# Kernel tuning notes

Hardware: AMD Instinct MI355X
Metric: run time of the kernel (lower is better)

The kernel has to match this reference:

```python
import jax, jax.numpy as jnp
import numpy as np

KEY_DIM, VALUE_DIM, NUM_HEAD, OUT_DIM = 128, 64, 4, 64
HEAD_KDIM = KEY_DIM // NUM_HEAD   # 32
HEAD_VDIM = VALUE_DIM // NUM_HEAD # 16

def _xavier(key, shape):
    # xavier_uniform over (fan_in=shape[0], fan_out=prod(shape[1:])) like torch
    fan_in, fan_out = shape[0], int(np.prod(shape[1:]))
    lim = float(np.sqrt(6.0 / (fan_in + fan_out)))
    return jax.random.uniform(key, shape, jnp.float32, -lim, lim)

def setup_inputs() -> dict:
    key = jax.random.key(0)
    ks = jax.random.split(key, 7)
    B, Q, K = 2, 4096, 4096
    return {
        "q_data": jax.random.normal(ks[0], (B, Q, KEY_DIM), jnp.float32),
        "m_data": jax.random.normal(ks[1], (B, K, VALUE_DIM), jnp.float32),
        "mask": jax.random.randint(ks[2], (B, K), 0, 2, jnp.int32),
        "q_weights": _xavier(ks[3], (KEY_DIM, NUM_HEAD, HEAD_KDIM)),
        "k_weights": _xavier(ks[4], (VALUE_DIM, NUM_HEAD, HEAD_KDIM)),
        "v_weights": _xavier(ks[5], (VALUE_DIM, NUM_HEAD, HEAD_VDIM)),
        "o_weights": _xavier(ks[6], (NUM_HEAD, HEAD_VDIM, OUT_DIM)),
        "o_bias": jnp.zeros((OUT_DIM,), jnp.float32),
    }

def reference(q_data, m_data, mask, q_weights, k_weights, v_weights, o_weights, o_bias):
    head_kdim = q_weights.shape[-1]
    scale = head_kdim ** (-0.5)
    Q = jnp.einsum('bqa,ahc->bqhc', q_data, q_weights) * scale
    K = jnp.einsum('bka,ahc->bkhc', m_data, k_weights)
    V = jnp.einsum('bka,ahc->bkhc', m_data, v_weights)
    logits = jnp.einsum('bqhc,bkhc->bhqk', Q, K)
    neg = jnp.finfo(logits.dtype).min
    logits = jnp.where(mask[:, None, None, :] == 0, neg, logits)
    weights = jax.nn.softmax(logits, axis=-1)
    weight_avg = jnp.einsum('bhqk,bkhc->bqhc', weights, V)
    return jnp.einsum('bqhc,hco->bqo', weight_avg, o_weights) + o_bias
```

## Files before the change

kernel.cpp:

```cpp
#include <hip/hip_runtime.h>
#include <stdint.h>

#define B_  2
#define QN  4096
#define KN  4096
#define AD  128
#define MD  64
#define H_  4
#define C_  32
#define CV  16
#define OD  64

typedef short bf16x8 __attribute__((ext_vector_type(8)));
typedef short bf16x4 __attribute__((ext_vector_type(4)));
typedef float f32x4  __attribute__((ext_vector_type(4)));

__device__ __forceinline__ short f2bf(float f) {
  union { float f; unsigned u; } v; v.f = f;
  unsigned r = v.u + 0x7fffu + ((v.u >> 16) & 1u);
  return (short)(r >> 16);
}
__device__ __forceinline__ unsigned pack2t(float a, float b) {
  union { float f; unsigned u; } ua, ub; ua.f = a; ub.f = b;
  return __builtin_amdgcn_perm(ub.u, ua.u, 0x07060302u);
}
__device__ __forceinline__ bf16x4 pack4t(f32x4 p) {
  union { unsigned u[2]; bf16x4 v; } t;
  t.u[0] = pack2t(p[0], p[1]); t.u[1] = pack2t(p[2], p[3]);
  return t.v;
}
__device__ __forceinline__ bf16x8 cvt8(f32x4 a, f32x4 b) {
  bf16x8 o;
  o[0]=f2bf(a[0]); o[1]=f2bf(a[1]); o[2]=f2bf(a[2]); o[3]=f2bf(a[3]);
  o[4]=f2bf(b[0]); o[5]=f2bf(b[1]); o[6]=f2bf(b[2]); o[7]=f2bf(b[3]);
  return o;
}

__global__ __launch_bounds__(256) void k_proj(const float* __restrict__ qdf, const float* __restrict__ mdf,
                                              const float* __restrict__ qwf, const float* __restrict__ kwf,
                                              const float* __restrict__ vwf,
                                              const int* __restrict__ mask, int* __restrict__ kc,
                                              short* __restrict__ Qp, short* __restrict__ Kp,
                                              short* __restrict__ Vpt) {
  const int lane = threadIdx.x & 63;
  const int wid = threadIdx.x >> 6;
  const int n = lane & 15, quad = lane >> 4;
  const f32x4 z4 = {0.f,0.f,0.f,0.f};
  if (blockIdx.x < 1024) {
    const int t = blockIdx.x*4 + wid;
    const int rt = t >> 3, ct = t & 7;
    const int row = rt*16 + n;
    const int hc0 = ct*16;
    f32x4 acc = z4;
    #pragma unroll
    for (int ak = 0; ak < 4; ++ak) {
      const int a0 = ak*32 + quad*8;
      const float* ap = qdf + row*AD + a0;
      bf16x8 afrag = cvt8(*(const f32x4*)ap, *(const f32x4*)(ap + 4));
      bf16x8 bfrag;
      #pragma unroll
      for (int j = 0; j < 8; ++j) bfrag[j] = f2bf(qwf[(a0 + j)*128 + hc0 + n]);
      acc = __builtin_amdgcn_mfma_f32_16x16x32_bf16(afrag, bfrag, acc, 0, 0, 0);
    }
    const int h = hc0 >> 5, c0 = (hc0 & 31) + n;
    const float s = 0.17677669529663687f * 1.44269504088896341f;
    #pragma unroll
    for (int r = 0; r < 4; ++r) {
      const int rr = rt*16 + quad*4 + r;
      const int bb = rr >> 12, q = rr & 4095;
      Qp[((bb*H_ + h)*QN + q)*C_ + c0] = f2bf(acc[r] * s);
    }
    return;
  }
  __shared__ unsigned long long balS[64];
  __shared__ int pref[64];
  __shared__ int kcS;
  const int bidx = blockIdx.x - 1024;
  const int b = (bidx*4) / 3072;
  #pragma unroll
  for (int p = 0; p < 16; ++p) {
    const int seg = wid*16 + p;
    const unsigned long long bal = __ballot(mask[b*KN + seg*64 + lane] != 0);
    if (lane == 0) balS[seg] = bal;
  }
  __syncthreads();
  if (wid == 0) {
    int v = __popcll(balS[lane]); int incl = v;
    for (int d = 1; d < 64; d <<= 1) { int o = __shfl_up(incl, d); if (lane >= d) incl += o; }
    pref[lane] = incl - v;
    if (lane == 63) kcS = incl;
  }
  __syncthreads();
  const int Kc = kcS;
  const int nch = (Kc + 31) >> 5;
  const int t = bidx*4 + wid;
  const int rem = t - b*3072;
  const int rt = rem / 12, ct = rem - rt*12;
  if (rem == 0 && lane == 0) kc[b] = Kc;
  if (rt*16 >= nch*32) return;
  const int j = rt*16 + n;
  const int valid = (j < Kc);
  int src = 0;
  if (valid) {
    int seg = 0;
    #pragma unroll
    for (int st = 32; st >= 1; st >>= 1)
      if (seg + st < 64 && pref[seg + st] <= j) seg += st;
    int r2 = j - pref[seg];
    unsigned long long m = balS[seg];
    int pos = 0;
    #pragma unroll
    for (int w = 32; w >= 1; w >>= 1) {
      const int c = __popcll(m & ((1ull << w) - 1ull));
      if (r2 >= c) { r2 -= c; m >>= w; pos += w; }
    }
    src = seg*64 + pos;
  }
  const float* mrow = mdf + (b*KN + src)*MD;
  const int hc = ct*16 + n;
  f32x4 acc = z4;
  #pragma unroll
  for (int ch = 0; ch < 2; ++ch) {
    const int a0 = ch*32 + quad*8;
    bf16x8 afrag = cvt8(*(const f32x4*)(mrow + a0), *(const f32x4*)(mrow + a0 + 4));
    if (!valid) {
      #pragma unroll
      for (int jj = 0; jj < 8; ++jj) afrag[jj] = 0;
    }
    bf16x8 bfrag;
    if (ct < 8) {
      #pragma unroll
      for (int jj = 0; jj < 8; ++jj) bfrag[jj] = f2bf(kwf[(a0 + jj)*128 + hc]);
    } else {
      #pragma unroll
      for (int jj = 0; jj < 8; ++jj) bfrag[jj] = f2bf(vwf[(a0 + jj)*64 + hc - 128]);
    }
    acc = __builtin_amdgcn_mfma_f32_16x16x32_bf16(afrag, bfrag, acc, 0, 0, 0);
  }
  if (ct < 8) {
    const int h = hc >> 5, c = hc & 31;
    #pragma unroll
    for (int r = 0; r < 4; ++r) {
      const int jj2 = rt*16 + quad*4 + r;
      Kp[((b*H_ + h)*KN + jj2)*C_ + c] = f2bf(acc[r]);
    }
  } else {
    const int hc2 = hc - 128; const int h = hc2 >> 4, cv = hc2 & 15;
    bf16x4 pk; pk[0]=f2bf(acc[0]); pk[1]=f2bf(acc[1]); pk[2]=f2bf(acc[2]); pk[3]=f2bf(acc[3]);
    *(bf16x4*)(Vpt + ((b*H_ + h)*CV + cv)*KN + rt*16 + quad*4) = pk;
  }
}

__global__ __launch_bounds__(1024) void k_attn(const short* __restrict__ Qp, const short* __restrict__ Kp,
                                               const short* __restrict__ Vpt, const int* __restrict__ kc,
                                               const float* __restrict__ w2f, const float* __restrict__ obf,
                                               float* __restrict__ out) {
  __shared__ __attribute__((aligned(16))) char pool[40960];
  const int lane = threadIdx.x & 63, wid = threadIdx.x >> 6;
  const int h = wid & 3, split = wid >> 2;
  const int flatq = blockIdx.x * 32;
  const int b = flatq >> 12, qt = flatq & 4095;
  const int bh = b*H_ + h;
  const int n = lane & 15, quad = lane >> 4;
  const short* Qb = Qp + (bh*QN + qt)*C_;
  const short* Kb = Kp + bh*KN*C_;
  const short* Vb = Vpt + bh*CV*KN;
  const bf16x8 qb0 = *(const bf16x8*)(Qb + n*C_ + quad*8);
  const bf16x8 qb1 = *(const bf16x8*)(Qb + (16 + n)*C_ + quad*8);
  const int Kc = kc[b];
  const int nch = (Kc + 31) >> 5;
  const f32x4 z4 = {0.f,0.f,0.f,0.f};
  f32x4 o0 = z4, o1 = z4;
  float l0 = 0.f, l1 = 0.f;
  short* Pw = (short*)(pool + wid*2560);
  bf16x8 kf0, kf1, va;
  int ci = split;
  if (ci < nch) {
    const int kb = ci*32;
    kf0 = *(const bf16x8*)(Kb + (kb + n)*C_ + quad*8);
    kf1 = *(const bf16x8*)(Kb + (kb + 16 + n)*C_ + quad*8);
    va  = *(const bf16x8*)(Vb + n*KN + kb + quad*8);
  }
  for (; ci < nch; ci += 4) {
    const bf16x8 ckf0 = kf0, ckf1 = kf1, cva = va;
    const int cin = ci + 4;
    if (cin < nch) {
      const int kb2 = cin*32;
      kf0 = *(const bf16x8*)(Kb + (kb2 + n)*C_ + quad*8);
      kf1 = *(const bf16x8*)(Kb + (kb2 + 16 + n)*C_ + quad*8);
      va  = *(const bf16x8*)(Vb + n*KN + kb2 + quad*8);
    }
    f32x4 s00 = __builtin_amdgcn_mfma_f32_16x16x32_bf16(ckf0, qb0, z4, 0, 0, 0);
    f32x4 s01 = __builtin_amdgcn_mfma_f32_16x16x32_bf16(ckf0, qb1, z4, 0, 0, 0);
    f32x4 s10 = __builtin_amdgcn_mfma_f32_16x16x32_bf16(ckf1, qb0, z4, 0, 0, 0);
    f32x4 s11 = __builtin_amdgcn_mfma_f32_16x16x32_bf16(ckf1, qb1, z4, 0, 0, 0);
    f32x4 p00, p01, p10, p11;
    #pragma unroll
    for (int r = 0; r < 4; ++r) {
      p00[r] = __builtin_amdgcn_exp2f(s00[r]);
      p01[r] = __builtin_amdgcn_exp2f(s01[r]);
      p10[r] = __builtin_amdgcn_exp2f(s10[r]);
      p11[r] = __builtin_amdgcn_exp2f(s11[r]);
    }
    l0 += ((p00[0]+p00[1])+(p00[2]+p00[3])) + ((p10[0]+p10[1])+(p10[2]+p10[3]));
    l1 += ((p01[0]+p01[1])+(p01[2]+p01[3])) + ((p11[0]+p11[1])+(p11[2]+p11[3]));
    *(bf16x4*)(Pw + n*40 + quad*4)           = pack4t(p00);
    *(bf16x4*)(Pw + n*40 + 16 + quad*4)      = pack4t(p10);
    *(bf16x4*)(Pw + (16+n)*40 + quad*4)      = pack4t(p01);
    *(bf16x4*)(Pw + (16+n)*40 + 16 + quad*4) = pack4t(p11);
    const bf16x8 pb0 = *(const bf16x8*)(Pw + n*40 + quad*8);
    const bf16x8 pb1 = *(const bf16x8*)(Pw + (16+n)*40 + quad*8);
    o0 = __builtin_amdgcn_mfma_f32_16x16x32_bf16(cva, pb0, o0, 0, 0, 0);
    o1 = __builtin_amdgcn_mfma_f32_16x16x32_bf16(cva, pb1, o1, 0, 0, 0);
  }
  __syncthreads();
  float* Of   = (float*)pool;
  float* Lb   = (float*)(pool + 33280);
  short* ObfA = (short*)(pool + 35328);
  #pragma unroll
  for (int r = 0; r < 4; ++r) {
    const int hc = h*16 + quad*4 + r;
    Of[split*2080 + n*65 + hc]        = o0[r];
    Of[split*2080 + (16+n)*65 + hc]   = o1[r];
  }
  l0 += __shfl_xor(l0, 16); l0 += __shfl_xor(l0, 32);
  l1 += __shfl_xor(l1, 16); l1 += __shfl_xor(l1, 32);
  if (lane < 16) {
    Lb[split*128 + h*32 + lane]      = l0;
    Lb[split*128 + h*32 + 16 + lane] = l1;
  }
  __syncthreads();
  {
    const float npad = (float)(nch*32 - Kc);
    const int e = threadIdx.x * 2;
    const int q = e >> 6, hc = e & 63;
    const int hh = hc >> 4;
    const float l = (Lb[hh*32 + q] + Lb[128 + hh*32 + q])
                  + (Lb[256 + hh*32 + q] + Lb[384 + hh*32 + q]) - npad;
    const float inv = 1.00135f / l;
    const float v0 = ((Of[q*65 + hc]     + Of[2080 + q*65 + hc])
                    + (Of[4160 + q*65 + hc] + Of[6240 + q*65 + hc])) * inv;
    const float v1 = ((Of[q*65 + hc + 1] + Of[2080 + q*65 + hc + 1])
                    + (Of[4160 + q*65 + hc + 1] + Of[6240 + q*65 + hc + 1])) * inv;
    union { unsigned u; short s[2]; } pk;
    pk.s[0] = f2bf(v0); pk.s[1] = f2bf(v1);
    *(unsigned*)(ObfA + q*72 + hc) = pk.u;
  }
  __syncthreads();
  if (wid < 8) {
    const int mt = wid & 1, nt = wid >> 1;
    f32x4 acc = z4;
    #pragma unroll
    for (int kchunk = 0; kchunk < 2; ++kchunk) {
      const bf16x8 afrag = *(const bf16x8*)(ObfA + (mt*16 + n)*72 + kchunk*32 + quad*8);
      bf16x8 bfrag;
      #pragma unroll
      for (int jj = 0; jj < 8; ++jj)
        bfrag[jj] = f2bf(w2f[(kchunk*32 + quad*8 + jj)*64 + nt*16 + n]);
      acc = __builtin_amdgcn_mfma_f32_16x16x32_bf16(afrag, bfrag, acc, 0, 0, 0);
    }
    const int ocol = nt*16 + n;
    const float bias = obf[ocol];
    #pragma unroll
    for (int r = 0; r < 4; ++r) {
      const int qg = flatq + mt*16 + quad*4 + r;
      out[qg*64 + ocol] = acc[r] + bias;
    }
  }
}

extern "C" void kernel_launch(void* const* d_in, const int* in_sizes, int n_in,
                              void* d_out, int out_size, void* d_ws, size_t ws_size,
                              hipStream_t stream) {
  const float* qd  = (const float*)d_in[0];
  const float* md  = (const float*)d_in[1];
  const int*   msk = (const int*)  d_in[2];
  const float* qw  = (const float*)d_in[3];
  const float* kw  = (const float*)d_in[4];
  const float* vw  = (const float*)d_in[5];
  const float* ow  = (const float*)d_in[6];
  const float* ob  = (const float*)d_in[7];
  float* out = (float*)d_out;

  char* ws = (char*)d_ws;
  int*   kc  = (int*)  (ws);
  short* Qp  = (short*)(ws + (64<<10));
  short* Kp  = (short*)(ws + (64<<10) + (2u<<20));
  short* Vpt = (short*)(ws + (64<<10) + (4u<<20));

  hipLaunchKernelGGL(k_proj, dim3(2560), dim3(256),  0, stream, qd, md, qw, kw, vw, msk, kc, Qp, Kp, Vpt);
  hipLaunchKernelGGL(k_attn, dim3(256),  dim3(1024), 0, stream, Qp, Kp, Vpt, kc, ow, ob, out);
}
```

Before: 103.2 us.

## Fuse projection and attention into one cooperative kernel with grid sync

Measured after the change: 145.9 us. +41.5%, slower.

```diff
diff --git a/kernel.cpp b/kernel.cpp
--- a/kernel.cpp
+++ b/kernel.cpp
@@ -1,4 +1,5 @@
 #include <hip/hip_runtime.h>
+#include <hip/hip_cooperative_groups.h>
 #include <stdint.h>
 
 #define B_  2
@@ -36,21 +37,34 @@
   return o;
 }
 
-__global__ __launch_bounds__(256) void k_proj(const float* __restrict__ qdf, const float* __restrict__ mdf,
-                                              const float* __restrict__ qwf, const float* __restrict__ kwf,
-                                              const float* __restrict__ vwf,
-                                              const int* __restrict__ mask, int* __restrict__ kc,
-                                              short* __restrict__ Qp, short* __restrict__ Kp,
-                                              short* __restrict__ Vpt) {
-  const int lane = threadIdx.x & 63;
-  const int wid = threadIdx.x >> 6;
+__global__ __launch_bounds__(1024) void k_fused(
+    const float* __restrict__ qdf, const float* __restrict__ mdf,
+    const float* __restrict__ qwf, const float* __restrict__ kwf,
+    const float* __restrict__ vwf, const int* __restrict__ mask,
+    short* __restrict__ Kp, short* __restrict__ Vpt,
+    const float* __restrict__ w2f, const float* __restrict__ obf,
+    float* __restrict__ out) {
+  __shared__ __attribute__((aligned(16))) char pool[40960];
+  __shared__ __attribute__((aligned(16))) short QL[32*136];
+  __shared__ unsigned long long balS[64];
+  __shared__ int pref[64];
+  __shared__ int kcS;
+  const int lane = threadIdx.x & 63, wid = threadIdx.x >> 6;
   const int n = lane & 15, quad = lane >> 4;
+  const int bid = blockIdx.x;
+  const int flatq = bid * 32;
+  const int b = bid >> 7;
   const f32x4 z4 = {0.f,0.f,0.f,0.f};
-  if (blockIdx.x < 1024) {
-    const int t = blockIdx.x*4 + wid;
-    const int rt = t >> 3, ct = t & 7;
-    const int row = rt*16 + n;
-    const int hc0 = ct*16;
+
+  #pragma unroll
+  for (int p = 0; p < 4; ++p) {
+    const int seg = wid*4 + p;
+    const unsigned long long bal = __ballot(mask[b*KN + seg*64 + lane] != 0);
+    if (lane == 0) balS[seg] = bal;
+  }
+  {
+    const int mt = wid & 1, ct = wid >> 1;
+    const int row = flatq + mt*16 + n;
     f32x4 acc = z4;
     #pragma unroll
     for (int ak = 0; ak < 4; ++ak) {
@@ -59,29 +73,13 @@
       bf16x8 afrag = cvt8(*(const f32x4*)ap, *(const f32x4*)(ap + 4));
       bf16x8 bfrag;
       #pragma unroll
-      for (int j = 0; j < 8; ++j) bfrag[j] = f2bf(qwf[(a0 + j)*128 + hc0 + n]);
+      for (int j = 0; j < 8; ++j) bfrag[j] = f2bf(qwf[(a0 + j)*128 + ct*16 + n]);
       acc = __builtin_amdgcn_mfma_f32_16x16x32_bf16(afrag, bfrag, acc, 0, 0, 0);
     }
-    const int h = hc0 >> 5, c0 = (hc0 & 31) + n;
     const float s = 0.17677669529663687f * 1.44269504088896341f;
     #pragma unroll
-    for (int r = 0; r < 4; ++r) {
-      const int rr = rt*16 + quad*4 + r;
-      const int bb = rr >> 12, q = rr & 4095;
-      Qp[((bb*H_ + h)*QN + q)*C_ + c0] = f2bf(acc[r] * s);
-    }
-    return;
-  }
-  __shared__ unsigned long long balS[64];
-  __shared__ int pref[64];
-  __shared__ int kcS;
-  const int bidx = blockIdx.x - 1024;
-  const int b = (bidx*4) / 3072;
-  #pragma unroll
-  for (int p = 0; p < 16; ++p) {
-    const int seg = wid*16 + p;
-    const unsigned long long bal = __ballot(mask[b*KN + seg*64 + lane] != 0);
-    if (lane == 0) balS[seg] = bal;
+    for (int r = 0; r < 4; ++r)
+      QL[(mt*16 + quad*4 + r)*136 + ct*16 + n] = f2bf(acc[r] * s);
   }
   __syncthreads();
   if (wid == 0) {
@@ -93,83 +91,69 @@
   __syncthreads();
   const int Kc = kcS;
   const int nch = (Kc + 31) >> 5;
-  const int t = bidx*4 + wid;
-  const int rem = t - b*3072;
-  const int rt = rem / 12, ct = rem - rt*12;
-  if (rem == 0 && lane == 0) kc[b] = Kc;
-  if (rt*16 >= nch*32) return;
-  const int j = rt*16 + n;
-  const int valid = (j < Kc);
-  int src = 0;
-  if (valid) {
-    int seg = 0;
-    #pragma unroll
-    for (int st = 32; st >= 1; st >>= 1)
-      if (seg + st < 64 && pref[seg + st] <= j) seg += st;
-    int r2 = j - pref[seg];
-    unsigned long long m = balS[seg];
-    int pos = 0;
-    #pragma unroll
-    for (int w = 32; w >= 1; w >>= 1) {
-      const int c = __popcll(m & ((1ull << w) - 1ull));
-      if (r2 >= c) { r2 -= c; m >>= w; pos += w; }
-    }
-    src = seg*64 + pos;
-  }
-  const float* mrow = mdf + (b*KN + src)*MD;
-  const int hc = ct*16 + n;
-  f32x4 acc = z4;
-  #pragma unroll
-  for (int ch = 0; ch < 2; ++ch) {
-    const int a0 = ch*32 + quad*8;
-    bf16x8 afrag = cvt8(*(const f32x4*)(mrow + a0), *(const f32x4*)(mrow + a0 + 4));
-    if (!valid) {
-      #pragma unroll
-      for (int jj = 0; jj < 8; ++jj) afrag[jj] = 0;
-    }
-    bf16x8 bfrag;
-    if (ct < 8) {
-      #pragma unroll
-      for (int jj = 0; jj < 8; ++jj) bfrag[jj] = f2bf(kwf[(a0 + jj)*128 + hc]);
+  for (int tt = wid; tt < 24; tt += 16) {
+    const int t = (bid & 127)*24 + tt;
+    const int rt = t / 12, ctk = t - rt*12;
+    if (rt*16 >= nch*32) continue;
+    const int j = rt*16 + n;
+    const int valid = (j < Kc);
+    int src = 0;
+    if (valid) {
+      int seg = 0;
+      #pragma unroll
+      for (int st = 32; st >= 1; st >>= 1)
+        if (seg + st < 64 && pref[seg + st] <= j) seg += st;
+      int r2 = j - pref[seg];
+      unsigned long long m = balS[seg];
+      int pos = 0;
+      #pragma unroll
+      for (int w = 32; w >= 1; w >>= 1) {
+        const int c = __popcll(m & ((1ull << w) - 1ull));
+        if (r2 >= c) { r2 -= c; m >>= w; pos += w; }
+      }
+      src = seg*64 + pos;
+    }
+    const float* mrow = mdf + (b*KN + src)*MD;
+    const int hc = ctk*16 + n;
+    f32x4 acc = z4;
+    #pragma unroll
+    for (int ch = 0; ch < 2; ++ch) {
+      const int a0 = ch*32 + quad*8;
+      bf16x8 afrag = cvt8(*(const f32x4*)(mrow + a0), *(const f32x4*)(mrow + a0 + 4));
+      if (!valid) {
+        #pragma unroll
+        for (int jj = 0; jj < 8; ++jj) afrag[jj] = 0;
+      }
+      bf16x8 bfrag;
+      if (ctk < 8) {
+        #pragma unroll
+        for (int jj = 0; jj < 8; ++jj) bfrag[jj] = f2bf(kwf[(a0 + jj)*128 + hc]);
+      } else {
+        #pragma unroll
+        for (int jj = 0; jj < 8; ++jj) bfrag[jj] = f2bf(vwf[(a0 + jj)*64 + hc - 128]);
+      }
+      acc = __builtin_amdgcn_mfma_f32_16x16x32_bf16(afrag, bfrag, acc, 0, 0, 0);
+    }
+    if (ctk < 8) {
+      const int h = hc >> 5, c = hc & 31;
+      #pragma unroll
+      for (int r = 0; r < 4; ++r) {
+        const int jj2 = rt*16 + quad*4 + r;
+        Kp[((b*H_ + h)*KN + jj2)*C_ + c] = f2bf(acc[r]);
+      }
     } else {
-      #pragma unroll
-      for (int jj = 0; jj < 8; ++jj) bfrag[jj] = f2bf(vwf[(a0 + jj)*64 + hc - 128]);
-    }
-    acc = __builtin_amdgcn_mfma_f32_16x16x32_bf16(afrag, bfrag, acc, 0, 0, 0);
-  }
-  if (ct < 8) {
-    const int h = hc >> 5, c = hc & 31;
-    #pragma unroll
-    for (int r = 0; r < 4; ++r) {
-      const int jj2 = rt*16 + quad*4 + r;
-      Kp[((b*H_ + h)*KN + jj2)*C_ + c] = f2bf(acc[r]);
-    }
-  } else {
-    const int hc2 = hc - 128; const int h = hc2 >> 4, cv = hc2 & 15;
-    bf16x4 pk; pk[0]=f2bf(acc[0]); pk[1]=f2bf(acc[1]); pk[2]=f2bf(acc[2]); pk[3]=f2bf(acc[3]);
-    *(bf16x4*)(Vpt + ((b*H_ + h)*CV + cv)*KN + rt*16 + quad*4) = pk;
-  }
-}
-
-__global__ __launch_bounds__(1024) void k_attn(const short* __restrict__ Qp, const short* __restrict__ Kp,
-                                               const short* __restrict__ Vpt, const int* __restrict__ kc,
-                                               const float* __restrict__ w2f, const float* __restrict__ obf,
-                                               float* __restrict__ out) {
-  __shared__ __attribute__((aligned(16))) char pool[40960];
-  const int lane = threadIdx.x & 63, wid = threadIdx.x >> 6;
+      const int hc2 = hc - 128; const int h = hc2 >> 4, cv = hc2 & 15;
+      bf16x4 pk; pk[0]=f2bf(acc[0]); pk[1]=f2bf(acc[1]); pk[2]=f2bf(acc[2]); pk[3]=f2bf(acc[3]);
+      *(bf16x4*)(Vpt + ((b*H_ + h)*CV + cv)*KN + rt*16 + quad*4) = pk;
+    }
+  }
+  cooperative_groups::this_grid().sync();
   const int h = wid & 3, split = wid >> 2;
-  const int flatq = blockIdx.x * 32;
-  const int b = flatq >> 12, qt = flatq & 4095;
   const int bh = b*H_ + h;
-  const int n = lane & 15, quad = lane >> 4;
-  const short* Qb = Qp + (bh*QN + qt)*C_;
   const short* Kb = Kp + bh*KN*C_;
   const short* Vb = Vpt + bh*CV*KN;
-  const bf16x8 qb0 = *(const bf16x8*)(Qb + n*C_ + quad*8);
-  const bf16x8 qb1 = *(const bf16x8*)(Qb + (16 + n)*C_ + quad*8);
-  const int Kc = kc[b];
-  const int nch = (Kc + 31) >> 5;
-  const f32x4 z4 = {0.f,0.f,0.f,0.f};
+  const bf16x8 qb0 = *(const bf16x8*)(QL + n*136 + h*32 + quad*8);
+  const bf16x8 qb1 = *(const bf16x8*)(QL + (16 + n)*136 + h*32 + quad*8);
   f32x4 o0 = z4, o1 = z4;
   float l0 = 0.f, l1 = 0.f;
   short* Pw = (short*)(pool + wid*2560);
@@ -220,8 +204,8 @@
   #pragma unroll
   for (int r = 0; r < 4; ++r) {
     const int hc = h*16 + quad*4 + r;
-    Of[split*2080 + n*65 + hc]        = o0[r];
-    Of[split*2080 + (16+n)*65 + hc]   = o1[r];
+    Of[split*2080 + n*65 + hc]      = o0[r];
+    Of[split*2080 + (16+n)*65 + hc] = o1[r];
   }
   l0 += __shfl_xor(l0, 16); l0 += __shfl_xor(l0, 32);
   l1 += __shfl_xor(l1, 16); l1 += __shfl_xor(l1, 32);
@@ -283,11 +267,11 @@
   float* out = (float*)d_out;
 
   char* ws = (char*)d_ws;
-  int*   kc  = (int*)  (ws);
-  short* Qp  = (short*)(ws + (64<<10));
-  short* Kp  = (short*)(ws + (64<<10) + (2u<<20));
-  short* Vpt = (short*)(ws + (64<<10) + (4u<<20));
-
-  hipLaunchKernelGGL(k_proj, dim3(2560), dim3(256),  0, stream, qd, md, qw, kw, vw, msk, kc, Qp, Kp, Vpt);
-  hipLaunchKernelGGL(k_attn, dim3(256),  dim3(1024), 0, stream, Qp, Kp, Vpt, kc, ow, ob, out);
-}
+  short* Kp  = (short*)(ws);
+  short* Vpt = (short*)(ws + (2u<<20));
+
+  void* args[] = { (void*)&qd, (void*)&md, (void*)&qw, (void*)&kw, (void*)&vw,
+                   (void*)&msk, (void*)&Kp, (void*)&Vpt, (void*)&ow, (void*)&ob,
+                   (void*)&out };
+  hipLaunchCooperativeKernel((const void*)k_fused, dim3(256), dim3(1024), args, 0, stream);
+}
```
